# Optimization experiments

Hardware: AMD Instinct MI355X
Metric: run time of the kernel (lower is better)

The kernel has to match this reference:

```python
import jax, jax.numpy as jnp
import numpy as np

D, H, T, K = 512, 8, 4, 64   # dim, n_heads, n_tasks, topk_n
HD = D // H
PRUNE, EPS = 1e-3, 1e-8


def _ln(x, g, b, eps=1e-5):
    m = jnp.mean(x, axis=-1, keepdims=True)
    v = jnp.mean((x - m) ** 2, axis=-1, keepdims=True)
    return (x - m) * jax.lax.rsqrt(v + eps) * g + b


def setup_inputs() -> dict:
    key = jax.random.key(0)
    ks = jax.random.split(key, 5)
    B, N = 16, 8192
    tokens = jax.random.normal(ks[0], (B, N, D), jnp.float32)
    key_padding_mask = jax.random.uniform(ks[1], (B, N)) < 0.1  # True marks padding
    q = jax.random.normal(ks[2], (1, T, D), jnp.float32) * 0.02
    in_proj_w = jax.random.normal(ks[3], (3 * D, D), jnp.float32) / np.sqrt(D).astype(np.float32)
    in_proj_b = jnp.zeros((3 * D,), jnp.float32)
    pre_g = jnp.ones((D,), jnp.float32)
    pre_b = jnp.zeros((D,), jnp.float32)
    q_g = jnp.ones((D,), jnp.float32)
    q_b = jnp.zeros((D,), jnp.float32)
    log_tau = jnp.asarray(np.log(0.3), jnp.float32)
    return dict(tokens=tokens, key_padding_mask=key_padding_mask, q=q,
                in_proj_w=in_proj_w, in_proj_b=in_proj_b,
                pre_g=pre_g, pre_b=pre_b, q_g=q_g, q_b=q_b, log_tau=log_tau)


def reference(tokens, key_padding_mask, q, in_proj_w, in_proj_b,
              pre_g, pre_b, q_g, q_b, log_tau):
    B, N, _ = tokens.shape
    kpm = key_padding_mask  # [B,N], True = pad

    normed = _ln(tokens, pre_g, pre_b)                       # [B,N,D]
    tau = jnp.clip(jnp.exp(log_tau), 0.1, 10.0)
    query = _ln(q, q_g, q_b) / tau                           # [1,T,D]

    wq, wk, wv = in_proj_w[:D], in_proj_w[D:2 * D], in_proj_w[2 * D:]
    bq, bk, bv = in_proj_b[:D], in_proj_b[D:2 * D], in_proj_b[2 * D:]

    qp = (query[0] @ wq.T + bq).reshape(T, H, HD)            # [T,H,hd]
    kp = (normed @ wk.T + bk).reshape(B, N, H, HD)           # [B,N,H,hd]

    scores = jnp.einsum('thd,bnhd->bhtn', qp, kp) / np.float32(np.sqrt(HD))
    scores = jnp.where(kpm[:, None, None, :], -jnp.inf, scores)
    attn = jax.nn.softmax(scores, axis=-1)                   # [B,H,T,N]

    alpha = attn.mean(axis=1)                                # [B,T,N]
    alpha = jnp.where(kpm[:, None, :], 0.0, alpha)
    alpha = alpha / jnp.maximum(alpha.sum(-1, keepdims=True), EPS)

    # prune below threshold, with argmax one-hot fallback if everything pruned
    a = jnp.where(alpha < PRUNE, 0.0, alpha)
    a = jnp.where(kpm[:, None, :], 0.0, a)
    s = a.sum(-1, keepdims=True)
    need_fallback = s <= EPS                                 # [B,T,1]
    base = jnp.where(kpm[:, None, :], -1.0, alpha)
    onehot = jax.nn.one_hot(jnp.argmax(base, axis=-1), N, dtype=a.dtype)  # [B,T,N]
    a = jnp.where(need_fallback, onehot, a)
    a = jnp.where(kpm[:, None, :], 0.0, a)
    alpha = a / jnp.maximum(a.sum(-1, keepdims=True), EPS)

    # pool source: tie_mha_v projection of normed inputs
    pool_source = normed @ wv.T + bv                         # [B,N,D]

    # top-k gather + renorm weighting
    topv, topi = jax.lax.top_k(alpha, K)                     # [B,T,K]
    selected = jnp.take_along_axis(pool_source[:, None, :, :], topi[..., None], axis=2)  # [B,T,K,D]
    w = topv / jnp.maximum(topv.sum(-1, keepdims=True), EPS)
    pooled = (w[..., None] * selected).sum(axis=2)           # [B,T,D]
    return pooled
```

## Files before the change

kernel.cpp:

```cpp
#include <hip/hip_runtime.h>
#include <math.h>

#define Dd   512
#define Hh   8
#define Tt   4
#define HDd  64
#define Bb   16
#define Nn   8192
#define HTc  32
#define KS   64
#define NTOK (Bb*Nn)
#define PRUNEc 0.001f
#define EPSc   1e-8f

#define WS_C1     0u
#define WS_C0     128u
#define WS_M      2048u
#define WS_L      4096u
#define WS_TOPW   6144u
#define WS_TOPI   22528u
#define WS_FLAG   38912u
#define WS_G2H    65536u
#define WS_G2M    98304u
#define WS_G2L    131072u
#define WS_MEAN   163840u
#define WS_INV    688128u
#define WS_MASK8  1212416u
#define WS_SCORES 2097152u

typedef __attribute__((ext_vector_type(8)))  short short8v;
typedef __attribute__((ext_vector_type(16))) float f32x16;

__device__ __forceinline__ void split3(float x, unsigned &h, unsigned &m, unsigned &l){
  unsigned u  = __float_as_uint(x);
  unsigned uh = u & 0xFFFF0000u;
  float rh = x - __uint_as_float(uh);
  unsigned um = __float_as_uint(rh) & 0xFFFF0000u;
  float rm = rh - __uint_as_float(um);
  unsigned ul = __float_as_uint(rm) & 0xFFFF0000u;
  h = uh; m = um; l = ul;
}

__global__ void tap_detect(const unsigned* mraw, int* flag){
  int tid = threadIdx.x;
  if (tid == 0) *flag = 0;
  __syncthreads();
  int f = 0;
  for (int i = tid; i < NTOK/4; i += 256){
    unsigned v = mraw[i];
    if (v == 0x3f800000u) f |= 2;
    else if (v & ~1u)     f |= 1;
  }
  if (f) atomicOr(flag, f);
}

__global__ void tap_mask(const void* mraw, const int* flag, unsigned char* m8){
  int i = blockIdx.x*256 + threadIdx.x;
  int fl = *flag;
  unsigned char m;
  if (fl & 2)      m = (((const float*)mraw)[i] != 0.0f);
  else if (fl & 1) m = (((const unsigned char*)mraw)[i] != 0);
  else             m = (((const int*)mraw)[i] != 0);
  m8[i] = m;
}

__global__ void tap_prep(const float* q, const float* ipw, const float* ipb,
                         const float* pre_g, const float* pre_b,
                         const float* q_g, const float* q_b, const float* log_tau,
                         unsigned short* G2h, unsigned short* G2m, unsigned short* G2l,
                         float* C1, float* C0){
  __shared__ float query[Tt][Dd];
  __shared__ float qps[HDd];
  __shared__ float red[256];
  int tid = threadIdx.x;
  int ht = blockIdx.x;
  int h = ht >> 2, t = ht & 3;
  float tau = expf(log_tau[0]);
  tau = fminf(fmaxf(tau, 0.1f), 10.0f);
  float itau = 1.0f / tau;
  int wv = tid >> 6, lane = tid & 63;
  {
    const float* qr = q + wv*Dd;
    float s = 0.f, ss = 0.f;
    for (int j = lane; j < Dd; j += 64){ float x = qr[j]; s += x; ss += x*x; }
    #pragma unroll
    for (int off = 32; off; off >>= 1){ s += __shfl_down(s, off); ss += __shfl_down(ss, off); }
    s = __shfl(s, 0); ss = __shfl(ss, 0);
    float mean = s * (1.f/Dd);
    float var  = ss * (1.f/Dd) - mean*mean;
    float inv  = rsqrtf(var + 1e-5f);
    for (int j = lane; j < Dd; j += 64){
      float x = qr[j];
      query[wv][j] = ((x - mean)*inv*q_g[j] + q_b[j]) * itau;
    }
  }
  __syncthreads();
  {
    int d = tid >> 2, sub = tid & 3;
    int i = h*HDd + d;
    const float* wrow = ipw + (size_t)i*Dd;
    float acc = 0.f;
    int j0 = sub*128;
    for (int j = 0; j < 128; ++j) acc += query[t][j0+j]*wrow[j0+j];
    red[tid] = acc;
    __syncthreads();
    if (sub == 0) qps[d] = red[tid]+red[tid+1]+red[tid+2]+red[tid+3] + ipb[i];
    __syncthreads();
  }
  float c1p = 0.f, c0p = 0.f;
  for (int jj = 0; jj < 2; ++jj){
    int j = tid + jj*256;
    float acc = 0.f;
    #pragma unroll 8
    for (int d = 0; d < HDd; ++d)
      acc += qps[d] * ipw[(size_t)(Dd + h*HDd + d)*Dd + j];
    float w2 = acc * 0.125f;
    float g2 = w2 * pre_g[j];
    unsigned uh, um, ul;
    split3(g2, uh, um, ul);
    G2h[ht*Dd + j] = (unsigned short)(uh >> 16);
    G2m[ht*Dd + j] = (unsigned short)(um >> 16);
    G2l[ht*Dd + j] = (unsigned short)(ul >> 16);
    float geff = __uint_as_float(uh) + __uint_as_float(um) + __uint_as_float(ul);
    c1p += geff;
    c0p += w2 * pre_b[j];
  }
  if (tid < HDd) c0p += qps[tid] * ipb[Dd + h*HDd + tid] * 0.125f;
  red[tid] = c1p; __syncthreads();
  for (int s = 128; s; s >>= 1){ if (tid < s) red[tid] += red[tid+s]; __syncthreads(); }
  if (tid == 0) C1[ht] = red[0];
  __syncthreads();
  red[tid] = c0p; __syncthreads();
  for (int s = 128; s; s >>= 1){ if (tid < s) red[tid] += red[tid+s]; __syncthreads(); }
  if (tid == 0) C0[ht] = red[0];
}

__global__ __launch_bounds__(256, 2) void tap_scores(
    const float* __restrict__ tokens,
    const unsigned short* __restrict__ G2h, const unsigned short* __restrict__ G2m,
    const unsigned short* __restrict__ G2l,
    const float* __restrict__ C1, const float* __restrict__ C0,
    float* __restrict__ scores, float* __restrict__ meanw, float* __restrict__ invw){
  __shared__ __align__(16) unsigned short xh[128*64];
  __shared__ __align__(16) unsigned short xm[128*64];
  __shared__ __align__(16) unsigned short xl[128*64];
  __shared__ float smean[128], sinv[128];
  __shared__ float c1s[32], c0s[32];
  int tid  = threadIdx.x;
  int lane = tid & 63, wv = tid >> 6;
  size_t t0 = (size_t)blockIdx.x * 128;
  if (tid < 32){ c1s[tid] = C1[tid]; c0s[tid] = C0[tid]; }

  f32x16 acc;
  #pragma unroll
  for (int i = 0; i < 16; ++i) acc[i] = 0.f;

  int trow = tid >> 4;
  int tcol = tid & 15;
  int brow  = (wv << 5) | (lane & 31);
  int bhalf = lane >> 5;
  const float4* tokv = (const float4*)(tokens + t0*(size_t)Dd);
  float ps[8], pss[8];
  #pragma unroll
  for (int i = 0; i < 8; ++i){ ps[i] = 0.f; pss[i] = 0.f; }

  for (int c = 0; c < 8; ++c){
    __syncthreads();
    #pragma unroll
    for (int i = 0; i < 8; ++i){
      int row = trow + (i << 4);
      float4 v = tokv[(size_t)row*128 + c*16 + tcol];
      ps[i]  += v.x + v.y + v.z + v.w;
      pss[i] += v.x*v.x + v.y*v.y + v.z*v.z + v.w*v.w;
      unsigned h0,m0,l0,h1,m1,l1,h2,m2,l2,h3,m3,l3;
      split3(v.x, h0, m0, l0); split3(v.y, h1, m1, l1);
      split3(v.z, h2, m2, l2); split3(v.w, h3, m3, l3);
      int off = row*128 + (((tcol << 3)) ^ ((row & 7) << 4));
      *(uint2*)((char*)xh + off) = make_uint2((h0>>16)|(h1&0xFFFF0000u), (h2>>16)|(h3&0xFFFF0000u));
      *(uint2*)((char*)xm + off) = make_uint2((m0>>16)|(m1&0xFFFF0000u), (m2>>16)|(m3&0xFFFF0000u));
      *(uint2*)((char*)xl + off) = make_uint2((l0>>16)|(l1&0xFFFF0000u), (l2>>16)|(l3&0xFFFF0000u));
    }
    __syncthreads();
    #pragma unroll
    for (int kc = 0; kc < 4; ++kc){
      int boff = brow*128 + ((((kc << 5) | (bhalf << 4))) ^ ((brow & 7) << 4));
      short8v bh = *(const short8v*)((const char*)xh + boff);
      short8v bm = *(const short8v*)((const char*)xm + boff);
      short8v bl = *(const short8v*)((const char*)xl + boff);
      int gi = ((lane & 31) << 9) | (c << 6) | (kc << 4) | (bhalf << 3);
      short8v ah = *(const short8v*)(G2h + gi);
      short8v am = *(const short8v*)(G2m + gi);
      short8v al = *(const short8v*)(G2l + gi);
      acc = __builtin_amdgcn_mfma_f32_32x32x16_bf16(ah, bh, acc, 0, 0, 0);
      acc = __builtin_amdgcn_mfma_f32_32x32x16_bf16(am, bh, acc, 0, 0, 0);
      acc = __builtin_amdgcn_mfma_f32_32x32x16_bf16(ah, bm, acc, 0, 0, 0);
      acc = __builtin_amdgcn_mfma_f32_32x32x16_bf16(am, bm, acc, 0, 0, 0);
      acc = __builtin_amdgcn_mfma_f32_32x32x16_bf16(al, bh, acc, 0, 0, 0);
      acc = __builtin_amdgcn_mfma_f32_32x32x16_bf16(ah, bl, acc, 0, 0, 0);
    }
  }
  #pragma unroll
  for (int i = 0; i < 8; ++i){
    float s = ps[i], ss = pss[i];
    #pragma unroll
    for (int off = 8; off; off >>= 1){
      s  += __shfl_down(s,  off, 16);
      ss += __shfl_down(ss, off, 16);
    }
    if (tcol == 0){
      int row = trow + (i << 4);
      float mean = s * (1.f/512.f);
      float var  = ss * (1.f/512.f) - mean*mean;
      float inv  = rsqrtf(var + 1e-5f);
      smean[row] = mean; sinv[row] = inv;
      meanw[t0 + row] = mean; invw[t0 + row] = inv;
    }
  }
  __syncthreads();
  float mean = smean[brow], inv = sinv[brow];
  int b = (int)(t0 >> 13);
  int n = (int)(t0 & 8191) + brow;
  #pragma unroll
  for (int r = 0; r < 16; ++r){
    int ht = (r & 3) + ((r >> 2) << 3) + ((lane >> 5) << 2);
    float sc = inv*(acc[r] - mean*c1s[ht]) + c0s[ht];
    scores[(((size_t)(b*HTc + ht)) << 13) + n] = sc;
  }
}

__global__ void tap_norm(const float* __restrict__ scores, const unsigned char* __restrict__ m8,
                         float* __restrict__ mrow, float* __restrict__ lrow){
  int R = blockIdx.x;
  int b = R >> 5;
  const float* srow = scores + (size_t)R*Nn;
  const unsigned char* mk = m8 + b*Nn;
  int tid = threadIdx.x;
  int wv = tid >> 6, lane = tid & 63;
  __shared__ float r4[4];
  float v[32];
  float mx = -1e30f;
  #pragma unroll
  for (int i = 0; i < 32; ++i){
    int n = tid + i*256;
    float s = srow[n];
    v[i] = mk[n] ? -1e30f : s;
    mx = fmaxf(mx, v[i]);
  }
  #pragma unroll
  for (int off = 32; off; off >>= 1) mx = fmaxf(mx, __shfl_down(mx, off));
  if (lane == 0) r4[wv] = mx;
  __syncthreads();
  mx = fmaxf(fmaxf(r4[0], r4[1]), fmaxf(r4[2], r4[3]));
  float se = 0.f;
  #pragma unroll
  for (int i = 0; i < 32; ++i) se += expf(v[i] - mx);
  #pragma unroll
  for (int off = 32; off; off >>= 1) se += __shfl_down(se, off);
  __syncthreads();
  if (lane == 0) r4[wv] = se;
  __syncthreads();
  if (tid == 0){ mrow[R] = mx; lrow[R] = r4[0]+r4[1]+r4[2]+r4[3]; }
}

__global__ void tap_alpha(const float* __restrict__ scores, const unsigned char* __restrict__ m8,
                          const float* __restrict__ mrow, const float* __restrict__ lrow,
                          float* __restrict__ topw, int* __restrict__ topi){
  __shared__ float av[Nn];
  __shared__ float lv[1024];
  __shared__ int   li[1024];
  __shared__ float rv[4]; __shared__ int ri[4]; __shared__ int rp[4];
  __shared__ int cnt; __shared__ int sArg;
  int bt = blockIdx.x;
  int b = bt >> 2, t = bt & 3;
  int tid = threadIdx.x;
  int wv = tid >> 6, lane = tid & 63;
  const unsigned char* mk = m8 + b*Nn;
  if (tid == 0) cnt = 0;
  float mh[Hh], il[Hh];
  const float* srows[Hh];
  #pragma unroll
  for (int h = 0; h < Hh; ++h){
    int R = b*HTc + h*Tt + t;
    mh[h] = mrow[R];
    il[h] = 1.0f / lrow[R];
    srows[h] = scores + (size_t)R*Nn;
  }
  float lsum = 0.f;
  float bvv = -2.f; int bii = 1<<30;
  for (int i = 0; i < 32; ++i){
    int n = tid + i*256;
    float a = 0.f;
    if (!mk[n]){
      #pragma unroll
      for (int h = 0; h < Hh; ++h) a += expf(srows[h][n] - mh[h]) * il[h];
      a *= 0.125f;
    }
    av[n] = a;
    lsum += a;
    float bb = mk[n] ? -1.f : a;
    if (bb > bvv || (bb == bvv && n < bii)){ bvv = bb; bii = n; }
  }
  #pragma unroll
  for (int off = 32; off; off >>= 1) lsum += __shfl_down(lsum, off);
  if (lane == 0) rv[wv] = lsum;
  __syncthreads();
  float Sall = rv[0]+rv[1]+rv[2]+rv[3];
  #pragma unroll
  for (int off = 32; off; off >>= 1){
    float ov = __shfl_down(bvv, off);
    int   oi = __shfl_down(bii, off);
    if (ov > bvv || (ov == bvv && oi < bii)){ bvv = ov; bii = oi; }
  }
  __syncthreads();
  if (lane == 0){ rv[wv] = bvv; ri[wv] = bii; }
  __syncthreads();
  if (tid == 0){
    float bv2 = rv[0]; int bi2 = ri[0];
    for (int w2 = 1; w2 < 4; ++w2)
      if (rv[w2] > bv2 || (rv[w2] == bv2 && ri[w2] < bi2)){ bv2 = rv[w2]; bi2 = ri[w2]; }
    sArg = bi2;
  }
  __syncthreads();
  float f1 = 1.0f / fmaxf(Sall, EPSc);
  for (int i = 0; i < 32; ++i){
    int n = tid + i*256;
    float x = av[n] * f1;
    if (x >= PRUNEc){
      int id = atomicAdd(&cnt, 1);
      if (id < 1024){ lv[id] = x; li[id] = n; }
    }
  }
  __syncthreads();
  int L = cnt;
  float* tw = topw + bt*KS;
  int*   ti = topi + bt*KS;
  if (L == 0){
    if (tid < KS){ tw[tid] = (tid == 0) ? 1.f : 0.f; ti[tid] = (tid == 0) ? sArg : 0; }
    return;
  }
  if (L <= KS){
    if (tid < KS){ tw[tid] = (tid < L) ? lv[tid] : 0.f; ti[tid] = (tid < L) ? li[tid] : 0; }
    return;
  }
  for (int k = 0; k < KS; ++k){
    float bv = -1.f; int bn = 1<<30; int bp = -1;
    for (int j = tid; j < L; j += 256){
      float x = lv[j]; int nn = li[j];
      if (x > bv || (x == bv && nn < bn)){ bv = x; bn = nn; bp = j; }
    }
    #pragma unroll
    for (int off = 32; off; off >>= 1){
      float ov = __shfl_down(bv, off);
      int   on = __shfl_down(bn, off);
      int   op = __shfl_down(bp, off);
      if (ov > bv || (ov == bv && on < bn)){ bv = ov; bn = on; bp = op; }
    }
    if (lane == 0){ rv[wv] = bv; ri[wv] = bn; rp[wv] = bp; }
    __syncthreads();
    if (tid == 0){
      float bb = rv[0]; int bj = ri[0]; int pp = rp[0];
      for (int w2 = 1; w2 < 4; ++w2)
        if (rv[w2] > bb || (rv[w2] == bb && ri[w2] < bj)){ bb = rv[w2]; bj = ri[w2]; pp = rp[w2]; }
      tw[k] = bb; ti[k] = bj;
      lv[pp] = -1.f;
    }
    __syncthreads();
  }
}

__global__ void tap_pool(const float* __restrict__ tokens, const float* __restrict__ ipw,
                         const float* __restrict__ ipb,
                         const float* __restrict__ pre_g, const float* __restrict__ pre_b,
                         const float* __restrict__ meanw, const float* __restrict__ invw,
                         const float* __restrict__ topw, const int* __restrict__ topi,
                         float* __restrict__ out){
  __shared__ float wk_[KS]; __shared__ int rk_[KS];
  __shared__ float coeff[KS];
  __shared__ __align__(16) float u[Dd];
  __shared__ float sW, sS;
  int bt = blockIdx.x;
  int b = bt >> 2;
  int tid = threadIdx.x;
  if (tid < KS){ wk_[tid] = topw[bt*KS + tid]; rk_[tid] = topi[bt*KS + tid]; }
  __syncthreads();
  if (tid < KS){
    float v = wk_[tid];
    #pragma unroll
    for (int off = 32; off; off >>= 1) v += __shfl_down(v, off);
    if (tid == 0) sW = v;
  }
  __syncthreads();
  float sumw = sW;
  float Winv = 1.0f / fmaxf(sumw, EPSc);
  float Wn   = sumw * Winv;
  if (tid < KS){
    int n = rk_[tid];
    float mk = meanw[(size_t)b*Nn + n];
    float ik = invw [(size_t)b*Nn + n];
    float wn = wk_[tid] * Winv;
    coeff[tid] = wn * ik;
    float sp = wn * mk * ik;
    #pragma unroll
    for (int off = 32; off; off >>= 1) sp += __shfl_down(sp, off);
    if (tid == 0) sS = sp;
  }
  __syncthreads();
  float Sv = sS;
  int d0 = tid, d1 = tid + 256;
  float acc0 = 0.f, acc1 = 0.f;
  #pragma unroll 4
  for (int k = 0; k < KS; ++k){
    float c = coeff[k];
    const float* xr = tokens + ((size_t)b*Nn + rk_[k])*Dd;
    acc0 = fmaf(c, xr[d0], acc0);
    acc1 = fmaf(c, xr[d1], acc1);
  }
  u[d0] = pre_g[d0]*(acc0 - Sv) + pre_b[d0]*Wn;
  u[d1] = pre_g[d1]*(acc1 - Sv) + pre_b[d1]*Wn;
  __syncthreads();
  const float4* u4 = (const float4*)u;
  const float4* w0 = (const float4*)(ipw + (size_t)(2*Dd + d0)*Dd);
  const float4* w1 = (const float4*)(ipw + (size_t)(2*Dd + d1)*Dd);
  float o0 = 0.f, o1 = 0.f;
  #pragma unroll 4
  for (int j4 = 0; j4 < 128; ++j4){
    float4 uu = u4[j4];
    float4 a = w0[j4], c = w1[j4];
    o0 += uu.x*a.x + uu.y*a.y + uu.z*a.z + uu.w*a.w;
    o1 += uu.x*c.x + uu.y*c.y + uu.z*c.z + uu.w*c.w;
  }
  out[bt*Dd + d0] = o0 + Wn*ipb[2*Dd + d0];
  out[bt*Dd + d1] = o1 + Wn*ipb[2*Dd + d1];
}

extern "C" void kernel_launch(void* const* d_in, const int* in_sizes, int n_in,
                              void* d_out, int out_size, void* d_ws, size_t ws_size,
                              hipStream_t stream){
  const float* tokens = (const float*)d_in[0];
  const void*  kpm    = d_in[1];
  const float* q      = (const float*)d_in[2];
  const float* ipw    = (const float*)d_in[3];
  const float* ipb    = (const float*)d_in[4];
  const float* pre_g  = (const float*)d_in[5];
  const float* pre_b  = (const float*)d_in[6];
  const float* q_g    = (const float*)d_in[7];
  const float* q_b    = (const float*)d_in[8];
  const float* ltau   = (const float*)d_in[9];
  char* ws = (char*)d_ws;
  float* C1    = (float*)(ws + WS_C1);
  float* C0    = (float*)(ws + WS_C0);
  float* mrow  = (float*)(ws + WS_M);
  float* lrow  = (float*)(ws + WS_L);
  float* topwv = (float*)(ws + WS_TOPW);
  int*   topiv = (int*)  (ws + WS_TOPI);
  int*   flag  = (int*)  (ws + WS_FLAG);
  unsigned short* G2h = (unsigned short*)(ws + WS_G2H);
  unsigned short* G2m = (unsigned short*)(ws + WS_G2M);
  unsigned short* G2l = (unsigned short*)(ws + WS_G2L);
  float* meanw = (float*)(ws + WS_MEAN);
  float* invw  = (float*)(ws + WS_INV);
  unsigned char* m8 = (unsigned char*)(ws + WS_MASK8);
  float* scores = (float*)(ws + WS_SCORES);
  float* out = (float*)d_out;

  hipLaunchKernelGGL(tap_detect, dim3(1), dim3(256), 0, stream, (const unsigned*)kpm, flag);
  hipLaunchKernelGGL(tap_mask,   dim3(NTOK/256), dim3(256), 0, stream, kpm, flag, m8);
  hipLaunchKernelGGL(tap_prep,   dim3(HTc), dim3(256), 0, stream,
                     q, ipw, ipb, pre_g, pre_b, q_g, q_b, ltau, G2h, G2m, G2l, C1, C0);
  hipLaunchKernelGGL(tap_scores, dim3(NTOK/128), dim3(256), 0, stream,
                     tokens, G2h, G2m, G2l, C1, C0, scores, meanw, invw);
  hipLaunchKernelGGL(tap_norm,   dim3(Bb*HTc), dim3(256), 0, stream, scores, m8, mrow, lrow);
  hipLaunchKernelGGL(tap_alpha,  dim3(Bb*Tt), dim3(256), 0, stream,
                     scores, m8, mrow, lrow, topwv, topiv);
  hipLaunchKernelGGL(tap_pool,   dim3(Bb*Tt), dim3(256), 0, stream,
                     tokens, ipw, ipb, pre_g, pre_b, meanw, invw, topwv, topiv, out);
}
```

Baseline: 670.6 us.

## Load token rows directly into MFMA registers, drop LDS staging in scores kernel

```diff
diff --git a/kernel.cpp b/kernel.cpp
--- a/kernel.cpp
+++ b/kernel.cpp
@@ -41,15 +41,34 @@
   h = uh; m = um; l = ul;
 }
 
-__global__ void tap_detect(const unsigned* mraw, int* flag){
+__device__ __forceinline__ void split3x8(float4 v0, float4 v1,
+                                         short8v &h, short8v &m, short8v &l){
+  union { short8v s; unsigned u[4]; } H, M, L;
+  float a[8] = {v0.x,v0.y,v0.z,v0.w,v1.x,v1.y,v1.z,v1.w};
+  #pragma unroll
+  for (int w = 0; w < 4; ++w){
+    unsigned ha, ma, la, hb, mb, lb;
+    split3(a[2*w],   ha, ma, la);
+    split3(a[2*w+1], hb, mb, lb);
+    H.u[w] = (ha>>16) | (hb & 0xFFFF0000u);
+    M.u[w] = (ma>>16) | (mb & 0xFFFF0000u);
+    L.u[w] = (la>>16) | (lb & 0xFFFF0000u);
+  }
+  h = H.s; m = M.s; l = L.s;
+}
+
+__device__ __forceinline__ int chkw(unsigned v){
+  return (v == 0x3f800000u) ? 2 : ((v & ~1u) ? 1 : 0);
+}
+__global__ void tap_detect(const uint4* mraw, int* flag){
   int tid = threadIdx.x;
   if (tid == 0) *flag = 0;
   __syncthreads();
   int f = 0;
-  for (int i = tid; i < NTOK/4; i += 256){
-    unsigned v = mraw[i];
-    if (v == 0x3f800000u) f |= 2;
-    else if (v & ~1u)     f |= 1;
+  #pragma unroll
+  for (int i = 0; i < 8; ++i){
+    uint4 v = mraw[tid + i*1024];
+    f |= chkw(v.x) | chkw(v.y) | chkw(v.z) | chkw(v.w);
   }
   if (f) atomicOr(flag, f);
 }
@@ -135,62 +154,41 @@
   if (tid == 0) C0[ht] = red[0];
 }
 
-__global__ __launch_bounds__(256, 2) void tap_scores(
+__global__ __launch_bounds__(256, 4) void tap_scores(
     const float* __restrict__ tokens,
     const unsigned short* __restrict__ G2h, const unsigned short* __restrict__ G2m,
     const unsigned short* __restrict__ G2l,
     const float* __restrict__ C1, const float* __restrict__ C0,
     float* __restrict__ scores, float* __restrict__ meanw, float* __restrict__ invw){
-  __shared__ __align__(16) unsigned short xh[128*64];
-  __shared__ __align__(16) unsigned short xm[128*64];
-  __shared__ __align__(16) unsigned short xl[128*64];
-  __shared__ float smean[128], sinv[128];
-  __shared__ float c1s[32], c0s[32];
-  int tid  = threadIdx.x;
-  int lane = tid & 63, wv = tid >> 6;
+  int tid   = threadIdx.x;
+  int lane  = tid & 63, wv = tid >> 6;
+  int col   = lane & 31;
+  int bhalf = lane >> 5;
   size_t t0 = (size_t)blockIdx.x * 128;
-  if (tid < 32){ c1s[tid] = C1[tid]; c0s[tid] = C0[tid]; }
+  int brow  = (wv << 5) | col;
+  const float* __restrict__ xrow = tokens + (t0 + brow)*(size_t)Dd;
+  int abase = (col << 9) | (bhalf << 3);
 
   f32x16 acc;
   #pragma unroll
   for (int i = 0; i < 16; ++i) acc[i] = 0.f;
-
-  int trow = tid >> 4;
-  int tcol = tid & 15;
-  int brow  = (wv << 5) | (lane & 31);
-  int bhalf = lane >> 5;
-  const float4* tokv = (const float4*)(tokens + t0*(size_t)Dd);
-  float ps[8], pss[8];
-  #pragma unroll
-  for (int i = 0; i < 8; ++i){ ps[i] = 0.f; pss[i] = 0.f; }
+  float ps = 0.f, pss = 0.f;
 
   for (int c = 0; c < 8; ++c){
-    __syncthreads();
-    #pragma unroll
-    for (int i = 0; i < 8; ++i){
-      int row = trow + (i << 4);
-      float4 v = tokv[(size_t)row*128 + c*16 + tcol];
-      ps[i]  += v.x + v.y + v.z + v.w;
-      pss[i] += v.x*v.x + v.y*v.y + v.z*v.z + v.w*v.w;
-      unsigned h0,m0,l0,h1,m1,l1,h2,m2,l2,h3,m3,l3;
-      split3(v.x, h0, m0, l0); split3(v.y, h1, m1, l1);
-      split3(v.z, h2, m2, l2); split3(v.w, h3, m3, l3);
-      int off = row*128 + (((tcol << 3)) ^ ((row & 7) << 4));
-      *(uint2*)((char*)xh + off) = make_uint2((h0>>16)|(h1&0xFFFF0000u), (h2>>16)|(h3&0xFFFF0000u));
-      *(uint2*)((char*)xm + off) = make_uint2((m0>>16)|(m1&0xFFFF0000u), (m2>>16)|(m3&0xFFFF0000u));
-      *(uint2*)((char*)xl + off) = make_uint2((l0>>16)|(l1&0xFFFF0000u), (l2>>16)|(l3&0xFFFF0000u));
-    }
-    __syncthreads();
     #pragma unroll
     for (int kc = 0; kc < 4; ++kc){
-      int boff = brow*128 + ((((kc << 5) | (bhalf << 4))) ^ ((brow & 7) << 4));
-      short8v bh = *(const short8v*)((const char*)xh + boff);
-      short8v bm = *(const short8v*)((const char*)xm + boff);
-      short8v bl = *(const short8v*)((const char*)xl + boff);
-      int gi = ((lane & 31) << 9) | (c << 6) | (kc << 4) | (bhalf << 3);
-      short8v ah = *(const short8v*)(G2h + gi);
-      short8v am = *(const short8v*)(G2m + gi);
-      short8v al = *(const short8v*)(G2l + gi);
+      int k0 = (c << 6) | (kc << 4) | (bhalf << 3);
+      float4 v0 = *(const float4*)(xrow + k0);
+      float4 v1 = *(const float4*)(xrow + k0 + 4);
+      int ga = abase + (c << 6) + (kc << 4);
+      short8v ah = *(const short8v*)(G2h + ga);
+      short8v am = *(const short8v*)(G2m + ga);
+      short8v al = *(const short8v*)(G2l + ga);
+      ps  += v0.x+v0.y+v0.z+v0.w + v1.x+v1.y+v1.z+v1.w;
+      pss += v0.x*v0.x+v0.y*v0.y+v0.z*v0.z+v0.w*v0.w
+           + v1.x*v1.x+v1.y*v1.y+v1.z*v1.z+v1.w*v1.w;
+      short8v bh, bm, bl;
+      split3x8(v0, v1, bh, bm, bl);
       acc = __builtin_amdgcn_mfma_f32_32x32x16_bf16(ah, bh, acc, 0, 0, 0);
       acc = __builtin_amdgcn_mfma_f32_32x32x16_bf16(am, bh, acc, 0, 0, 0);
       acc = __builtin_amdgcn_mfma_f32_32x32x16_bf16(ah, bm, acc, 0, 0, 0);
@@ -199,31 +197,18 @@
       acc = __builtin_amdgcn_mfma_f32_32x32x16_bf16(ah, bl, acc, 0, 0, 0);
     }
   }
-  #pragma unroll
-  for (int i = 0; i < 8; ++i){
-    float s = ps[i], ss = pss[i];
-    #pragma unroll
-    for (int off = 8; off; off >>= 1){
-      s  += __shfl_down(s,  off, 16);
-      ss += __shfl_down(ss, off, 16);
-    }
-    if (tcol == 0){
-      int row = trow + (i << 4);
-      float mean = s * (1.f/512.f);
-      float var  = ss * (1.f/512.f) - mean*mean;
-      float inv  = rsqrtf(var + 1e-5f);
-      smean[row] = mean; sinv[row] = inv;
-      meanw[t0 + row] = mean; invw[t0 + row] = inv;
-    }
-  }
-  __syncthreads();
-  float mean = smean[brow], inv = sinv[brow];
+  ps  += __shfl_xor(ps, 32);
+  pss += __shfl_xor(pss, 32);
+  float mean = ps * (1.f/512.f);
+  float var  = pss * (1.f/512.f) - mean*mean;
+  float inv  = rsqrtf(var + 1e-5f);
+  if (bhalf == 0){ meanw[t0 + brow] = mean; invw[t0 + brow] = inv; }
   int b = (int)(t0 >> 13);
   int n = (int)(t0 & 8191) + brow;
   #pragma unroll
   for (int r = 0; r < 16; ++r){
-    int ht = (r & 3) + ((r >> 2) << 3) + ((lane >> 5) << 2);
-    float sc = inv*(acc[r] - mean*c1s[ht]) + c0s[ht];
+    int ht = (r & 3) + ((r >> 2) << 3) + (bhalf << 2);
+    float sc = inv*(acc[r] - mean*C1[ht]) + C0[ht];
     scores[(((size_t)(b*HTc + ht)) << 13) + n] = sc;
   }
 }
@@ -463,7 +448,7 @@
   float* scores = (float*)(ws + WS_SCORES);
   float* out = (float*)d_out;
 
-  hipLaunchKernelGGL(tap_detect, dim3(1), dim3(256), 0, stream, (const unsigned*)kpm, flag);
+  hipLaunchKernelGGL(tap_detect, dim3(1), dim3(1024), 0, stream, (const uint4*)kpm, flag);
   hipLaunchKernelGGL(tap_mask,   dim3(NTOK/256), dim3(256), 0, stream, kpm, flag, m8);
   hipLaunchKernelGGL(tap_prep,   dim3(HTc), dim3(256), 0, stream,
                      q, ipw, ipb, pre_g, pre_b, q_g, q_b, ltau, G2h, G2m, G2l, C1, C0);
```

New measurement: 604.7 us. 9.8% less time.
